# Kernel tuning notes

Hardware: AMD Instinct MI355X
Metric: run time of the kernel (lower is better)

Reference implementation:

```python
import jax, jax.numpy as jnp
import numpy as np

COMMITMENT_COST = 0.25

def setup_inputs() -> dict:
    key = jax.random.key(0)
    k1, k2 = jax.random.split(key)
    z = jax.random.normal(k1, (32768, 512), dtype=jnp.float32)
    # codebook initialized uniform(-1/K, 1/K) as in the torch module
    K = 8192
    W = jax.random.uniform(k2, (K, 512), dtype=jnp.float32, minval=-1.0 / K, maxval=1.0 / K)
    return {"z": z, "W": W}

def reference(z, W):
    # z: [B, D], W: [K, D]
    # squared-distance expansion: ||z||^2 + ||w||^2 - 2 z.w
    d2 = (jnp.sum(z * z, axis=1, keepdims=True)
          + jnp.sum(W * W, axis=1)
          - 2.0 * jnp.einsum('bd,kd->bk', z, W))  # [B, K]
    indices = jnp.argmin(d2, axis=1)              # [B]
    z_q_raw = W[indices]                          # [B, D]
    e_latent_loss = jnp.mean((jax.lax.stop_gradient(z_q_raw) - z) ** 2)
    q_latent_loss = jnp.mean((z_q_raw - jax.lax.stop_gradient(z)) ** 2)
    vq_loss = q_latent_loss + COMMITMENT_COST * e_latent_loss
    # straight-through estimator
    z_q = z + jax.lax.stop_gradient(z_q_raw - z)
    return (z_q, indices, vq_loss)
```

## Files before the change

### kernel.cpp

```cpp
#include <hip/hip_runtime.h>
#include <stdint.h>


#define B_ROWS 32768
#define DIM    512
#define KCODES 8192
#define SUPERS 4
#define TILES  16

typedef short bhalf8_t __attribute__((ext_vector_type(8)));
typedef float f32x4_t  __attribute__((ext_vector_type(4)));

__device__ __forceinline__ float b2f(unsigned short u) {
    return __uint_as_float(((unsigned int)u) << 16);
}
__device__ __forceinline__ unsigned short f2b(float f) {
    unsigned int x = __float_as_uint(f);
    return (unsigned short)((x + 0x7FFFu + ((x >> 16) & 1u)) >> 16);
}
__device__ __forceinline__ void gl_lds16(const void* g, void* l) {
    __builtin_amdgcn_global_load_lds(
        (const __attribute__((address_space(1))) unsigned int*)g,
        (__attribute__((address_space(3))) unsigned int*)l, 16, 0, 0);
}

__global__ __launch_bounds__(256) void k_split(const float4* __restrict__ src,
                                               ushort4* __restrict__ dst, int n4) {
    int i = blockIdx.x * 256 + threadIdx.x;
    int stride = gridDim.x * 256;
    for (; i < n4; i += stride) {
        float4 v = src[i];
        ushort4 h;
        h.x = f2b(v.x); h.y = f2b(v.y); h.z = f2b(v.z); h.w = f2b(v.w);
        dst[i] = h;
    }
}

__global__ __launch_bounds__(256) void k_pairsq(const float* __restrict__ X,
                                                float* __restrict__ out, int nrows) {
    int wid = threadIdx.x >> 6, lane = threadIdx.x & 63;
    int r = blockIdx.x * 4 + wid;
    if (r >= nrows) return;
    int b = lane >> 3, j = lane & 7;
    float acc = 0.f;
    if (b < 4) {
        const float* x = X + (size_t)r * DIM + b * 128 + j;
        float v = x[0];
        acc = __fmul_rn(v, v);
        for (int i = 1; i < 16; i++) {
            float w = x[8 * i];
            acc = __fadd_rn(acc, __fmul_rn(w, w));
        }
    }
    float t = __fadd_rn(acc, __shfl_xor(acc, 1));
    t = __fadd_rn(t, __shfl_xor(t, 2));
    t = __fadd_rn(t, __shfl_xor(t, 4));
    float u = __fadd_rn(t, __shfl_xor(t, 8));
    u = __fadd_rn(u, __shfl_xor(u, 16));
    if (lane == 0) out[r] = u;
}

__device__ __forceinline__ void compute_slice(const unsigned char* ba,
                                              const unsigned char* bb,
                                              int lane, f32x4_t acc[4][4]) {
    bhalf8_t af[4], bf[4];
#pragma unroll
    for (int f = 0; f < 4; f++) {
        af[f] = *(const bhalf8_t*)(ba + f * 1024 + lane * 16);
        bf[f] = *(const bhalf8_t*)(bb + f * 1024 + lane * 16);
    }
#pragma unroll
    for (int fm = 0; fm < 4; fm++)
#pragma unroll
        for (int fn = 0; fn < 4; fn++)
            acc[fm][fn] = __builtin_amdgcn_mfma_f32_16x16x32_bf16(af[fm], bf[fn], acc[fm][fn], 0, 0, 0);
}

__global__ __launch_bounds__(256, 4) void k_argmin(const unsigned short* __restrict__ Zh,
                                                   const unsigned short* __restrict__ Wh,
                                                   const float* __restrict__ ww,
                                                   float2* __restrict__ part) {
    __shared__ alignas(16) unsigned char smem[32768];
    const int tid = threadIdx.x;
    const int lane = tid & 63, w = tid >> 6;
    const int wm = w >> 1, wn = w & 1;
    const int lane15 = lane & 15, q = lane >> 4;
    const int b = blockIdx.x;
    const int super = b & 3;
    const int rb = (b >> 2) * 128;

    const int rowO0 = ((tid >> 6) << 4) | (tid & 15);
    const int kO0   = ((tid >> 4) & 3) << 3;
    const int dst0  = tid * 16;

    uint32_t p1[4][4], p2[4][4];
#pragma unroll
    for (int i = 0; i < 4; i++)
#pragma unroll
        for (int jj = 0; jj < 4; jj++) { p1[i][jj] = 0xFFFFFFFFu; p2[i][jj] = 0xFFFFFFFFu; }

    for (int tl = 0; tl < TILES; ++tl) {
        const int nt = super * 2048 + tl * 128;
        f32x4_t acc[4][4];
#pragma unroll
        for (int i = 0; i < 4; i++)
#pragma unroll
            for (int jj = 0; jj < 4; jj++) acc[i][jj] = (f32x4_t){0.f, 0.f, 0.f, 0.f};

        for (int kb = 0; kb < DIM; kb += 32) {
            __syncthreads();
            const int kg = kb + kO0;
            gl_lds16(Zh + (size_t)(rb + rowO0) * DIM + kg,      smem + dst0);
            gl_lds16(Zh + (size_t)(rb + rowO0 + 64) * DIM + kg, smem + 4096 + dst0);
            gl_lds16(Wh + (size_t)(nt + rowO0) * DIM + kg,      smem + 8192 + dst0);
            gl_lds16(Wh + (size_t)(nt + rowO0 + 64) * DIM + kg, smem + 8192 + 4096 + dst0);
            __syncthreads();

            compute_slice(smem + wm * 4096, smem + 8192 + wn * 4096, lane, acc);
        }

        float cb[4];
#pragma unroll
        for (int fn = 0; fn < 4; fn++)
            cb[fn] = ww[nt + wn * 64 + fn * 16 + lane15] + 0.5f;
#pragma unroll
        for (int fm = 0; fm < 4; fm++)
#pragma unroll
            for (int r = 0; r < 4; r++)
#pragma unroll
                for (int fn = 0; fn < 4; fn++) {
                    float sv = fmaf(-2.0f, acc[fm][fn][r], cb[fn]);
                    uint32_t pk = (__float_as_uint(sv) & 0xFFFFFF80u) | (uint32_t)(tl * 4 + fn);
                    if (pk < p1[fm][r]) { p2[fm][r] = p1[fm][r]; p1[fm][r] = pk; }
                    else if (pk < p2[fm][r]) { p2[fm][r] = pk; }
                }
    }

    __syncthreads();
    uint32_t* keys = (uint32_t*)smem;
#pragma unroll
    for (int fm = 0; fm < 4; fm++)
#pragma unroll
        for (int r = 0; r < 4; r++) {
            int row = wm * 64 + fm * 16 + q * 4 + r;
            int slice = wn * 16 + lane15;
            keys[(row * 32 + slice) * 2 + 0] = p1[fm][r];
            keys[(row * 32 + slice) * 2 + 1] = p2[fm][r];
        }
    __syncthreads();
    if (tid < 128) {
        int row = tid;
        int rglob = rb + row;
        for (int s = 0; s < 4; s++) {
            uint32_t bk = 0xFFFFFFFFu; int be = 0;
            for (int e = 0; e < 64; e++) {
                uint32_t k = keys[row * 64 + e];
                if (k < bk) { bk = k; be = e; }
            }
            int slice = be >> 1;
            int id = (int)(bk & 127u);
            int n = super * 2048 + (id >> 2) * 128 + (slice >> 4) * 64 + (id & 3) * 16 + (slice & 15);
            part[((size_t)rglob * SUPERS + super) * 4 + s] =
                make_float2(__uint_as_float(bk), __int_as_float(n));
            keys[row * 64 + be] = 0xFFFFFFFFu;
        }
    }
}

__global__ __launch_bounds__(256) void k_exact(const float* __restrict__ Zf,
                                               const float* __restrict__ Wf,
                                               const float2* __restrict__ part,
                                               const float* __restrict__ zz,
                                               const float* __restrict__ ww,
                                               float* __restrict__ outf,
                                               float* __restrict__ lossp) {
    __shared__ float wsum[4];
    int wid = threadIdx.x >> 6, lane = threadIdx.x & 63;
    int r = blockIdx.x * 4 + wid;
    int c = lane >> 2, j = lane & 3;

    float2 P = part[((size_t)r * SUPERS + (c >> 2)) * 4 + (c & 3)];
    int n = __float_as_int(P.y);
    n = min(max(n, 0), KCODES - 1);

    const float* zp = Zf + (size_t)r * DIM + j;
    const float* wp = Wf + (size_t)n * DIM + j;
    float acc = 0.f;
    for (int i = 0; i < 128; i++)
        acc = __fadd_rn(acc, __fmul_rn(zp[4 * i], wp[4 * i]));
    float t = __fadd_rn(acc, __shfl_xor(acc, 1));
    t = __fadd_rn(t, __shfl_xor(t, 2));
    float dot = __shfl(t, c * 4);

    float t1 = __fadd_rn(zz[r], ww[n]);
    float t2 = __fmul_rn(2.0f, dot);
    float d2 = __fadd_rn(t1, -t2);

    float bd = (j == 0) ? d2 : 3.4e38f;
    int   bn = (j == 0) ? n  : 0x7FFFFFFF;
#pragma unroll
    for (int off = 32; off; off >>= 1) {
        float od = __shfl_xor(bd, off);
        int   on = __shfl_xor(bn, off);
        if (od < bd || (od == bd && on < bn)) { bd = od; bn = on; }
    }
    int idx = bn;

    float4 wa = *(const float4*)(Wf + (size_t)idx * DIM + lane * 8);
    float4 wb = *(const float4*)(Wf + (size_t)idx * DIM + lane * 8 + 4);
    float4 za = *(const float4*)(Zf + (size_t)r   * DIM + lane * 8);
    float4 zb = *(const float4*)(Zf + (size_t)r   * DIM + lane * 8 + 4);
    *(float4*)(outf + (size_t)r * DIM + lane * 8)     = wa;
    *(float4*)(outf + (size_t)r * DIM + lane * 8 + 4) = wb;
    float d0 = za.x - wa.x, d1 = za.y - wa.y, dd2 = za.z - wa.z, d3 = za.w - wa.w;
    float d4 = zb.x - wb.x, d5 = zb.y - wb.y, d6 = zb.z - wb.z, d7 = zb.w - wb.w;
    float ls = d0*d0 + d1*d1 + dd2*dd2 + d3*d3 + d4*d4 + d5*d5 + d6*d6 + d7*d7;
#pragma unroll
    for (int off = 32; off; off >>= 1) ls += __shfl_xor(ls, off);
    if (lane == 0) {
        outf[(size_t)B_ROWS * DIM + r] = (float)idx;
        wsum[wid] = ls;
    }
    __syncthreads();
    if (threadIdx.x == 0) lossp[blockIdx.x] = wsum[0] + wsum[1] + wsum[2] + wsum[3];
}

__global__ __launch_bounds__(256) void k_loss(const float* __restrict__ lossp,
                                              float* __restrict__ outf) {
    __shared__ float sm[256];
    float a = 0.f;
    for (int i = threadIdx.x; i < 8192; i += 256) a += lossp[i];
    sm[threadIdx.x] = a;
    __syncthreads();
    for (int s = 128; s; s >>= 1) {
        if (threadIdx.x < s) sm[threadIdx.x] += sm[threadIdx.x + s];
        __syncthreads();
    }
    if (threadIdx.x == 0)
        outf[(size_t)B_ROWS * DIM + B_ROWS] = 1.25f * sm[0] / 16777216.0f;
}

extern "C" void kernel_launch(void* const* d_in, const int* in_sizes, int n_in,
                              void* d_out, int out_size, void* d_ws, size_t ws_size,
                              hipStream_t stream) {
    (void)in_sizes; (void)n_in; (void)out_size; (void)ws_size;
    const float* Zf = (const float*)d_in[0];
    const float* Wf = (const float*)d_in[1];
    float* outf = (float*)d_out;

    unsigned short* Zh = (unsigned short*)d_out;
    unsigned short* Wh = (unsigned short*)((char*)d_out + (32ull << 20));

    float*  ww    = (float*)d_ws;
    float*  zz    = (float*)((char*)d_ws + 32768);
    float*  lossp = (float*)((char*)d_ws + 163840);
    float2* partp = (float2*)((char*)d_ws + 196608);

    k_split<<<1024, 256, 0, stream>>>((const float4*)Zf, (ushort4*)Zh, B_ROWS * DIM / 4);
    k_split<<<512,  256, 0, stream>>>((const float4*)Wf, (ushort4*)Wh, KCODES * DIM / 4);
    k_pairsq<<<KCODES / 4, 256, 0, stream>>>(Wf, ww, KCODES);
    k_pairsq<<<B_ROWS / 4, 256, 0, stream>>>(Zf, zz, B_ROWS);
    k_argmin<<<(B_ROWS / 128) * SUPERS, 256, 0, stream>>>(Zh, Wh, ww, partp);
    k_exact<<<B_ROWS / 4, 256, 0, stream>>>(Zf, Wf, partp, zz, ww, outf, lossp);
    k_loss<<<1, 256, 0, stream>>>(lossp, outf);
}
```

Measured before the change: 874.8 us.

## Keep Z row block resident in LDS and halve rows per block

The argmin kernel now loads its whole 64-row bf16 Z block into 64KB of LDS once, instead of reloading Z for every K slice of every codebook tile. Each block covers 64 rows instead of 128, so the grid doubles and each wave holds 2x4 accumulators instead of 4x4. This removes the repeated Z global traffic but halves MFMA work per W load, doubling total W tile traffic. The 72KB LDS footprint limits blocks per CU.

```diff
diff --git a/kernel.cpp b/kernel.cpp
--- a/kernel.cpp
+++ b/kernel.cpp
@@ -7,6 +7,7 @@
 #define KCODES 8192
 #define SUPERS 4
 #define TILES  16
+#define ZROWS  64
 
 typedef short bhalf8_t __attribute__((ext_vector_type(8)));
 typedef float f32x4_t  __attribute__((ext_vector_type(4)));
@@ -60,63 +61,74 @@
     if (lane == 0) out[r] = u;
 }
 
-__device__ __forceinline__ void compute_slice(const unsigned char* ba,
-                                              const unsigned char* bb,
-                                              int lane, f32x4_t acc[4][4]) {
-    bhalf8_t af[4], bf[4];
-#pragma unroll
-    for (int f = 0; f < 4; f++) {
-        af[f] = *(const bhalf8_t*)(ba + f * 1024 + lane * 16);
-        bf[f] = *(const bhalf8_t*)(bb + f * 1024 + lane * 16);
-    }
-#pragma unroll
-    for (int fm = 0; fm < 4; fm++)
-#pragma unroll
-        for (int fn = 0; fn < 4; fn++)
-            acc[fm][fn] = __builtin_amdgcn_mfma_f32_16x16x32_bf16(af[fm], bf[fn], acc[fm][fn], 0, 0, 0);
-}
-
-__global__ __launch_bounds__(256, 4) void k_argmin(const unsigned short* __restrict__ Zh,
-                                                   const unsigned short* __restrict__ Wh,
-                                                   const float* __restrict__ ww,
-                                                   float2* __restrict__ part) {
-    __shared__ alignas(16) unsigned char smem[32768];
+__global__ __launch_bounds__(256) void k_argmin(const unsigned short* __restrict__ Zh,
+                                                const unsigned short* __restrict__ Wh,
+                                                const float* __restrict__ ww,
+                                                float2* __restrict__ part) {
+    __shared__ alignas(16) unsigned char smem[73728];
     const int tid = threadIdx.x;
     const int lane = tid & 63, w = tid >> 6;
     const int wm = w >> 1, wn = w & 1;
     const int lane15 = lane & 15, q = lane >> 4;
     const int b = blockIdx.x;
     const int super = b & 3;
-    const int rb = (b >> 2) * 128;
+    const int rb = (b >> 2) * ZROWS;
+
+    unsigned char* zl = smem;
+    unsigned char* wl = smem + 65536;
+
+    {
+        const int m = tid & 15;
+        const int kseg8 = ((tid >> 4) & 3) << 3;
+#pragma unroll
+        for (int i = 0; i < 16; i++) {
+            const int s = i * 256 + tid;
+            const int ks = s >> 8;
+            const int g = (s >> 6) & 3;
+            gl_lds16(Zh + (size_t)(rb + g * 16 + m) * DIM + ks * 32 + kseg8,
+                     zl + s * 16);
+        }
+    }
 
     const int rowO0 = ((tid >> 6) << 4) | (tid & 15);
     const int kO0   = ((tid >> 4) & 3) << 3;
     const int dst0  = tid * 16;
 
-    uint32_t p1[4][4], p2[4][4];
-#pragma unroll
-    for (int i = 0; i < 4; i++)
+    uint32_t p1[2][4], p2[2][4];
+#pragma unroll
+    for (int i = 0; i < 2; i++)
 #pragma unroll
         for (int jj = 0; jj < 4; jj++) { p1[i][jj] = 0xFFFFFFFFu; p2[i][jj] = 0xFFFFFFFFu; }
+
+    __syncthreads();
 
     for (int tl = 0; tl < TILES; ++tl) {
         const int nt = super * 2048 + tl * 128;
-        f32x4_t acc[4][4];
-#pragma unroll
-        for (int i = 0; i < 4; i++)
+        f32x4_t acc[2][4];
+#pragma unroll
+        for (int i = 0; i < 2; i++)
 #pragma unroll
             for (int jj = 0; jj < 4; jj++) acc[i][jj] = (f32x4_t){0.f, 0.f, 0.f, 0.f};
 
-        for (int kb = 0; kb < DIM; kb += 32) {
+        for (int ks = 0; ks < 16; ++ks) {
             __syncthreads();
-            const int kg = kb + kO0;
-            gl_lds16(Zh + (size_t)(rb + rowO0) * DIM + kg,      smem + dst0);
-            gl_lds16(Zh + (size_t)(rb + rowO0 + 64) * DIM + kg, smem + 4096 + dst0);
-            gl_lds16(Wh + (size_t)(nt + rowO0) * DIM + kg,      smem + 8192 + dst0);
-            gl_lds16(Wh + (size_t)(nt + rowO0 + 64) * DIM + kg, smem + 8192 + 4096 + dst0);
+            const int kg = ks * 32 + kO0;
+            gl_lds16(Wh + (size_t)(nt + rowO0) * DIM + kg,      wl + dst0);
+            gl_lds16(Wh + (size_t)(nt + rowO0 + 64) * DIM + kg, wl + 4096 + dst0);
             __syncthreads();
 
-            compute_slice(smem + wm * 4096, smem + 8192 + wn * 4096, lane, acc);
+            bhalf8_t af[2], bf[4];
+#pragma unroll
+            for (int f = 0; f < 2; f++)
+                af[f] = *(const bhalf8_t*)(zl + ks * 4096 + (wm * 2 + f) * 1024 + lane * 16);
+#pragma unroll
+            for (int f = 0; f < 4; f++)
+                bf[f] = *(const bhalf8_t*)(wl + (wn * 4096 + f * 1024) + lane * 16);
+#pragma unroll
+            for (int fm = 0; fm < 2; fm++)
+#pragma unroll
+                for (int fn = 0; fn < 4; fn++)
+                    acc[fm][fn] = __builtin_amdgcn_mfma_f32_16x16x32_bf16(af[fm], bf[fn], acc[fm][fn], 0, 0, 0);
         }
 
         float cb[4];
@@ -124,7 +136,7 @@
         for (int fn = 0; fn < 4; fn++)
             cb[fn] = ww[nt + wn * 64 + fn * 16 + lane15] + 0.5f;
 #pragma unroll
-        for (int fm = 0; fm < 4; fm++)
+        for (int fm = 0; fm < 2; fm++)
 #pragma unroll
             for (int r = 0; r < 4; r++)
 #pragma unroll
@@ -139,16 +151,16 @@
     __syncthreads();
     uint32_t* keys = (uint32_t*)smem;
 #pragma unroll
-    for (int fm = 0; fm < 4; fm++)
+    for (int fm = 0; fm < 2; fm++)
 #pragma unroll
         for (int r = 0; r < 4; r++) {
-            int row = wm * 64 + fm * 16 + q * 4 + r;
+            int row = wm * 32 + fm * 16 + q * 4 + r;
             int slice = wn * 16 + lane15;
             keys[(row * 32 + slice) * 2 + 0] = p1[fm][r];
             keys[(row * 32 + slice) * 2 + 1] = p2[fm][r];
         }
     __syncthreads();
-    if (tid < 128) {
+    if (tid < ZROWS) {
         int row = tid;
         int rglob = rb + row;
         for (int s = 0; s < 4; s++) {
@@ -260,7 +272,7 @@
     k_split<<<512,  256, 0, stream>>>((const float4*)Wf, (ushort4*)Wh, KCODES * DIM / 4);
     k_pairsq<<<KCODES / 4, 256, 0, stream>>>(Wf, ww, KCODES);
     k_pairsq<<<B_ROWS / 4, 256, 0, stream>>>(Zf, zz, B_ROWS);
-    k_argmin<<<(B_ROWS / 128) * SUPERS, 256, 0, stream>>>(Zh, Wh, ww, partp);
+    k_argmin<<<(B_ROWS / ZROWS) * SUPERS, 256, 0, stream>>>(Zh, Wh, ww, partp);
     k_exact<<<B_ROWS / 4, 256, 0, stream>>>(Zf, Wf, partp, zz, ww, outf, lossp);
     k_loss<<<1, 256, 0, stream>>>(lossp, outf);
 }
```

After: 909.5 us. 1.04x slower.
